# Kernel tuning notes

Measured on AMD Instinct MI355X. Metric: run time of the kernel, lower is better.

## Reference

```python
import jax, jax.numpy as jnp
import numpy as np

ENC_H = 128
DEC_H = 256
DEC_STEPS = 10


def _gru_cell(x, h, Wih, Whh, bih, bhh):
    # PyTorch GRU cell, gate order (r, z, n)
    gi = x @ Wih.T + bih          # (B, 3H)
    gh = h @ Whh.T + bhh          # (B, 3H)
    H = h.shape[-1]
    ir, iz, inn = gi[:, :H], gi[:, H:2 * H], gi[:, 2 * H:]
    hr, hz, hn = gh[:, :H], gh[:, H:2 * H], gh[:, 2 * H:]
    r = jax.nn.sigmoid(ir + hr)
    z = jax.nn.sigmoid(iz + hz)
    n = jnp.tanh(inn + r * hn)
    return (1.0 - z) * n + z * h


def setup_inputs() -> dict:
    key = jax.random.key(0)
    ks = jax.random.split(key, 12)
    B, S = 4096, 128
    s = 0.1
    return {
        "x": jax.random.normal(ks[0], (B, S, 5), jnp.float32),
        "y": jax.random.normal(ks[1], (B, S, 1), jnp.float32),
        "enc_Wih": jax.random.normal(ks[2], (3 * ENC_H, 5), jnp.float32) * s,
        "enc_Whh": jax.random.normal(ks[3], (3 * ENC_H, ENC_H), jnp.float32) * s,
        "enc_bih": jax.random.normal(ks[4], (3 * ENC_H,), jnp.float32) * s,
        "enc_bhh": jax.random.normal(ks[5], (3 * ENC_H,), jnp.float32) * s,
        "dec_Wih": jax.random.normal(ks[6], (3 * DEC_H, ENC_H + 1), jnp.float32) * s,
        "dec_Whh": jax.random.normal(ks[7], (3 * DEC_H, DEC_H), jnp.float32) * s,
        "dec_bih": jax.random.normal(ks[8], (3 * DEC_H,), jnp.float32) * s,
        "dec_bhh": jax.random.normal(ks[9], (3 * DEC_H,), jnp.float32) * s,
        "lin_W": jax.random.normal(ks[10], (4, DEC_H), jnp.float32) * s,
        "lin_b": jax.random.normal(ks[11], (4,), jnp.float32) * s,
    }


def reference(x, y, enc_Wih, enc_Whh, enc_bih, enc_bhh,
              dec_Wih, dec_Whh, dec_bih, dec_bhh, lin_W, lin_b):
    B, S, _ = x.shape
    xs = jnp.transpose(x, (1, 0, 2))   # (S, B, 5)
    ys = jnp.transpose(y, (1, 0, 2))   # (S, B, 1)

    # Encoder: only the final hidden state (contex) is consumed downstream.
    h0 = jnp.zeros((B, ENC_H), x.dtype)

    def enc_step(h, xt):
        return _gru_cell(xt, h, enc_Wih, enc_Whh, enc_bih, enc_bhh), None

    contex, _ = jax.lax.scan(enc_step, h0, xs)   # (B, 128)

    # Decoder: initial hidden is ones (torch.ones_like(shape)), 10 steps.
    hdec0 = jnp.ones((B, DEC_H), x.dtype)

    def dec_step(h, yt):
        xt = jnp.concatenate([contex, yt], axis=-1)   # (B, 129)
        h2 = _gru_cell(xt, h, dec_Wih, dec_Whh, dec_bih, dec_bhh)
        out = h2 @ lin_W.T + lin_b                    # (B, 4)
        return h2, out

    _, outs = jax.lax.scan(dec_step, hdec0, ys[:DEC_STEPS])  # (10, B, 4)

    # res starts as ones; only first 10 rows written.
    res = jnp.ones((S, B, 4), x.dtype).at[:DEC_STEPS].set(outs)
    return jnp.transpose(res, (1, 0, 2))   # (B, S, 4)
```

## Files before the change

### kernel.cpp

```cpp
#include <hip/hip_runtime.h>

#define B_SZ 4096
#define S_SZ 128
#define XD 5
#define EH 128
#define DH 256
#define DSTEPS 10

typedef short v8s __attribute__((ext_vector_type(8)));
typedef float v4f __attribute__((ext_vector_type(4)));

__device__ __forceinline__ float bf2f(unsigned short u) {
    union { unsigned int i; float f; } v; v.i = ((unsigned int)u) << 16; return v.f;
}
__device__ __forceinline__ unsigned short f2bf(float f) {
    union { float f; unsigned int i; } v; v.f = f;
    unsigned int x = v.i;
    return (unsigned short)((x + 0x7FFFu + ((x >> 16) & 1u)) >> 16);
}
__device__ __forceinline__ float fexp2(float x) { return __builtin_amdgcn_exp2f(x); }
__device__ __forceinline__ float frcp(float x) { return __builtin_amdgcn_rcpf(x); }
__device__ __forceinline__ unsigned int cvt2bf(float lo, float hi) {
    unsigned int r;
    asm("v_cvt_pk_bf16_f32 %0, %1, %2" : "=v"(r) : "v"(lo), "v"(hi));
    return r;
}

#define SC_S (-1.44269504088896f)
#define SC_T ( 2.88539008177793f)

__global__ __launch_bounds__(256) void prep_kernel(
    const float* __restrict__ dWih,
    const float* __restrict__ dWhh,
    unsigned short* __restrict__ wihp,
    unsigned short* __restrict__ dWhh_bf)
{
    const int gsz = gridDim.x * 256;
    for (int i = blockIdx.x * 256 + threadIdx.x; i < 768 * 256; i += gsz) {
        const float sc = ((i >> 8) < 512) ? SC_S : SC_T;
        dWhh_bf[i] = f2bf(sc * dWhh[i]);
    }
    for (int i = blockIdx.x * 256 + threadIdx.x; i < 768 * 136; i += gsz) {
        int col = i / 136, k = i - col * 136;
        const float sc = (col < 512) ? SC_S : SC_T;
        wihp[i] = (k < 129) ? f2bf(sc * dWih[col * 129 + k]) : (unsigned short)0;
    }
}

__global__ __launch_bounds__(1024)
void fused_kernel(
    const float* __restrict__ x,
    const float* __restrict__ Wih32,
    const float* __restrict__ Whh32,
    const float* __restrict__ bih,
    const float* __restrict__ bhh,
    const float* __restrict__ dbih,
    const float* __restrict__ dbhh,
    const float* __restrict__ y,
    const unsigned short* __restrict__ wihp,
    const unsigned short* __restrict__ dWhh_bf,
    const float* __restrict__ linW,
    const float* __restrict__ linb,
    float* __restrict__ out)
{
    __shared__ __align__(16) char uni[118784];
    __shared__ unsigned short hb[2][16][136];
    __shared__ __align__(16) unsigned short zpad[8];
    __shared__ unsigned short hshf[32 * 16 * 8];
    __shared__ unsigned short lwf[32 * 16 * 8];
    __shared__ float ysh[16][DSTEPS];

    const int tid = threadIdx.x;
    const int bid = blockIdx.x;
    const int wv = tid >> 6;
    const int lane = tid & 63;
    const int n = lane & 15;
    const int kg = lane >> 4;
    const int r0 = bid * 16;

    {
        auto xs = (unsigned short (*)[16][8])uni;

        for (int i = tid; i < 2 * 16 * 136; i += 1024) ((unsigned short*)hb)[i] = 0;
        if (tid < 8) zpad[tid] = 0;
        for (int i = tid; i < 16 * S_SZ * 8; i += 1024) {
            int m = i >> 10;
            int rem = i & 1023;
            int t = rem >> 3;
            int j = rem & 7;
            unsigned short v = 0;
            if (j < XD) v = f2bf(x[(size_t)(r0 + m) * (S_SZ * XD) + t * XD + j]);
            else if (j == XD) v = 0x3F80;
            xs[t][m][j] = v;
        }

        const int colw = wv * 16 + n;
        v8s fw[3][4];
        v8s fx[3];
        float bhn = 0.f;
        if (wv < 8) {
            #pragma unroll
            for (int g = 0; g < 3; ++g) {
                const float sc = (g < 2) ? SC_S : SC_T;
                const int gcol = g * EH + colw;
                #pragma unroll
                for (int kt = 0; kt < 4; ++kt) {
                    const float* p = &Whh32[(size_t)gcol * EH + kt * 32 + kg * 8];
                    float4 lo = *(const float4*)p;
                    float4 hi = *(const float4*)(p + 4);
                    v8s f;
                    f[0] = (short)f2bf(sc * lo.x); f[1] = (short)f2bf(sc * lo.y);
                    f[2] = (short)f2bf(sc * lo.z); f[3] = (short)f2bf(sc * lo.w);
                    f[4] = (short)f2bf(sc * hi.x); f[5] = (short)f2bf(sc * hi.y);
                    f[6] = (short)f2bf(sc * hi.z); f[7] = (short)f2bf(sc * hi.w);
                    fw[g][kt] = f;
                }
                v8s t = {0, 0, 0, 0, 0, 0, 0, 0};
                if (kg == 0) {
                    const float* p = &Wih32[gcol * XD];
                    #pragma unroll
                    for (int j = 0; j < XD; ++j) t[j] = (short)f2bf(sc * p[j]);
                    float b = (g < 2) ? (sc * (bih[gcol] + bhh[gcol]))
                                      : (sc * bih[gcol]);
                    t[XD] = (short)f2bf(b);
                }
                fx[g] = t;
            }
            bhn = SC_T * bhh[2 * EH + colw];
        }

        const v4f vzero = {0.f, 0.f, 0.f, 0.f};
        float hst[4] = {0.f, 0.f, 0.f, 0.f};
        __syncthreads();

        #pragma unroll 2
        for (int t = 0; t < S_SZ; ++t) {
            const int p = t & 1;
            if (wv < 8) {
                v8s a[4];
                #pragma unroll
                for (int kt = 0; kt < 4; ++kt)
                    a[kt] = *(const v8s*)&hb[p][n][kt * 32 + kg * 8];
                const unsigned short* xsrc = (kg == 0) ? &xs[t][n][0] : &zpad[0];
                v8s ax = *(const v8s*)xsrc;

                v4f accr  = __builtin_amdgcn_mfma_f32_16x16x32_bf16(a[0], fw[0][0], vzero, 0, 0, 0);
                v4f accz  = __builtin_amdgcn_mfma_f32_16x16x32_bf16(a[0], fw[1][0], vzero, 0, 0, 0);
                v4f acchn = __builtin_amdgcn_mfma_f32_16x16x32_bf16(a[0], fw[2][0], vzero, 0, 0, 0);
                #pragma unroll
                for (int kt = 1; kt < 4; ++kt) {
                    accr  = __builtin_amdgcn_mfma_f32_16x16x32_bf16(a[kt], fw[0][kt], accr, 0, 0, 0);
                    accz  = __builtin_amdgcn_mfma_f32_16x16x32_bf16(a[kt], fw[1][kt], accz, 0, 0, 0);
                    acchn = __builtin_amdgcn_mfma_f32_16x16x32_bf16(a[kt], fw[2][kt], acchn, 0, 0, 0);
                }
                accr = __builtin_amdgcn_mfma_f32_16x16x32_bf16(ax, fx[0], accr, 0, 0, 0);
                accz = __builtin_amdgcn_mfma_f32_16x16x32_bf16(ax, fx[1], accz, 0, 0, 0);
                v4f accin = __builtin_amdgcn_mfma_f32_16x16x32_bf16(ax, fx[2], vzero, 0, 0, 0);

                float hnew[4];
                #pragma unroll
                for (int e = 0; e < 4; ++e) {
                    float r  = frcp(1.f + fexp2(accr[e]));
                    float z  = frcp(1.f + fexp2(accz[e]));
                    float nn = 1.f - 2.f * frcp(fexp2(accin[e] + r * (acchn[e] + bhn)) + 1.f);
                    float h  = nn + z * (hst[e] - nn);
                    hst[e] = h;
                    hnew[e] = h;
                }
                const unsigned int pk01 = cvt2bf(hnew[0], hnew[1]);
                const unsigned int pk23 = cvt2bf(hnew[2], hnew[3]);
                hb[1 - p][kg * 4 + 0][colw] = (unsigned short)(pk01 & 0xFFFFu);
                hb[1 - p][kg * 4 + 1][colw] = (unsigned short)(pk01 >> 16);
                hb[1 - p][kg * 4 + 2][colw] = (unsigned short)(pk23 & 0xFFFFu);
                hb[1 - p][kg * 4 + 3][colw] = (unsigned short)(pk23 >> 16);
            }
            __syncthreads();
        }
    }

    {
        const int w = wv;
        const int colb = w * 16;
        const int rb = r0;
        float* gwsh = (float*)uni;

        if (tid < 512) {
            int col = tid >> 5, kgrp = tid & 31;
            unsigned short v8[8];
            #pragma unroll
            for (int j = 0; j < 8; ++j)
                v8[j] = (col < 4) ? f2bf(linW[col * 256 + kgrp * 8 + j]) : (unsigned short)0;
            *(uint4*)&lwf[(kgrp * 16 + col) * 8] = *(uint4*)v8;
        }
        if (tid < 16 * DSTEPS) {
            int row = tid / DSTEPS, tt = tid - row * DSTEPS;
            ysh[row][tt] = y[(size_t)(rb + row) * S_SZ + tt];
        }
        for (int i = tid; i < 32 * 16 * 8; i += 1024) hshf[i] = 0x3F80;

        v8s fB[3][8];
        #pragma unroll
        for (int g = 0; g < 3; ++g)
            #pragma unroll
            for (int kt = 0; kt < 8; ++kt)
                fB[g][kt] = *(const v8s*)
                    &dWhh_bf[(size_t)(g * DH + colb + n) * DH + kt * 32 + kg * 8];

        const v4f vzero = {0.f, 0.f, 0.f, 0.f};
        v4f gi[3];
        #pragma unroll
        for (int g = 0; g < 3; ++g) gi[g] = vzero;

        #pragma unroll
        for (int kt = 0; kt < 4; ++kt) {
            v8s actex = *(const v8s*)&hb[0][n][kt * 32 + kg * 8];
            #pragma unroll
            for (int g = 0; g < 3; ++g) {
                v8s bw = *(const v8s*)
                    &wihp[(size_t)(g * DH + colb + n) * 136 + kt * 32 + kg * 8];
                gi[g] = __builtin_amdgcn_mfma_f32_16x16x32_bf16(bw, actex, gi[g], 0, 0, 0);
            }
        }

        #pragma unroll
        for (int g = 0; g < 3; ++g) {
            const float sc = (g < 2) ? SC_S : SC_T;
            #pragma unroll
            for (int e = 0; e < 4; ++e) {
                const int gcol = g * DH + colb + kg * 4 + e;
                gi[g][e] += sc * (dbih[gcol] + ((g < 2) ? dbhh[gcol] : 0.f));
                gwsh[tid * 29 + 12 + g * 4 + e] = bf2f(wihp[(size_t)gcol * 136 + 128]);
            }
            *(v4f*)&gwsh[tid * 29 + g * 4] = gi[g];
        }
        #pragma unroll
        for (int e = 0; e < 4; ++e)
            gwsh[tid * 29 + 24 + e] = SC_T * dbhh[2 * DH + colb + kg * 4 + e];

        float hprev[4] = {1.f, 1.f, 1.f, 1.f};
        __syncthreads();

        for (int t = 0; t < DSTEPS; ++t) {
            const float yv = ysh[n][t];

            v4f ar = vzero, az = vzero, an = vzero;
            #pragma unroll
            for (int kt = 0; kt < 8; ++kt) {
                v8s a = *(const v8s*)&hshf[((kt * 4 + kg) * 16 + n) * 8];
                ar = __builtin_amdgcn_mfma_f32_16x16x32_bf16(fB[0][kt], a, ar, 0, 0, 0);
                az = __builtin_amdgcn_mfma_f32_16x16x32_bf16(fB[1][kt], a, az, 0, 0, 0);
                an = __builtin_amdgcn_mfma_f32_16x16x32_bf16(fB[2][kt], a, an, 0, 0, 0);
            }
            __syncthreads();

            float hh[4];
            #pragma unroll
            for (int e = 0; e < 4; ++e) {
                const float giR = gwsh[tid * 29 + 0 + e];
                const float giZ = gwsh[tid * 29 + 4 + e];
                const float giN = gwsh[tid * 29 + 8 + e];
                const float wyR = gwsh[tid * 29 + 12 + e];
                const float wyZ = gwsh[tid * 29 + 16 + e];
                const float wyN = gwsh[tid * 29 + 20 + e];
                const float bN  = gwsh[tid * 29 + 24 + e];
                float r  = frcp(1.f + fexp2(giR + yv * wyR + ar[e]));
                float z  = frcp(1.f + fexp2(giZ + yv * wyZ + az[e]));
                float nn = 1.f - 2.f * frcp(
                    fexp2(giN + yv * wyN + r * (an[e] + bN)) + 1.f);
                float h  = nn + z * (hprev[e] - nn);
                hprev[e] = h;
                hh[e] = h;
            }
            const unsigned int p01 = cvt2bf(hh[0], hh[1]);
            const unsigned int p23 = cvt2bf(hh[2], hh[3]);
            const int base = colb + kg * 4;
            const int idx = (((base >> 3) * 16) + n) * 8 + (base & 7);
            *(uint2*)&hshf[idx] = (uint2){p01, p23};
            __syncthreads();

            if (w == t) {
                v4f o4 = vzero;
                #pragma unroll
                for (int kt = 0; kt < 8; ++kt) {
                    v8s a = *(const v8s*)&hshf[((kt * 4 + kg) * 16 + n) * 8];
                    v8s b = *(const v8s*)&lwf[((kt * 4 + kg) * 16 + n) * 8];
                    o4 = __builtin_amdgcn_mfma_f32_16x16x32_bf16(b, a, o4, 0, 0, 0);
                }
                if (kg == 0) {
                    const float4 lb4 = *(const float4*)linb;
                    float4 ov = {o4[0] + lb4.x, o4[1] + lb4.y, o4[2] + lb4.z, o4[3] + lb4.w};
                    *(float4*)&out[(size_t)(rb + n) * (S_SZ * 4) + t * 4] = ov;
                }
            }
        }

        for (int j = tid; j < 16 * 512; j += 1024) {
            int row = j >> 9, c = j & 511;
            if (c >= DSTEPS * 4) out[(size_t)(rb + row) * 512 + c] = 1.0f;
        }
    }
}

extern "C" void kernel_launch(void* const* d_in, const int* in_sizes, int n_in,
                              void* d_out, int out_size, void* d_ws, size_t ws_size,
                              hipStream_t stream)
{
    const float* x    = (const float*)d_in[0];
    const float* y    = (const float*)d_in[1];
    const float* eWih = (const float*)d_in[2];
    const float* eWhh = (const float*)d_in[3];
    const float* ebih = (const float*)d_in[4];
    const float* ebhh = (const float*)d_in[5];
    const float* dWih = (const float*)d_in[6];
    const float* dWhh = (const float*)d_in[7];
    const float* dbih = (const float*)d_in[8];
    const float* dbhh = (const float*)d_in[9];
    const float* linW = (const float*)d_in[10];
    const float* linb = (const float*)d_in[11];
    float* out = (float*)d_out;

    char* ws = (char*)d_ws;
    unsigned short* wihp    = (unsigned short*)(ws);
    unsigned short* dWhh_bf = (unsigned short*)(ws + 208896);

    prep_kernel<<<256, 256, 0, stream>>>(dWih, dWhh, wihp, dWhh_bf);
    fused_kernel<<<256, 1024, 0, stream>>>(x, eWih, eWhh, ebih, ebhh,
                                           dbih, dbhh, y, wihp, dWhh_bf,
                                           linW, linb, out);
}
```

Baseline: 208.1 us.

## Split fused encoder/decoder into separate 512-thread encoder and decoder kernels

The encoder now runs in its own 512-thread kernel, so the 8 idle waves of the 1024-thread block no longer wait at every one of the 128 per-step barriers. The decoder weight preparation is folded into the encoder kernel, which removes the separate prep launch. The encoder writes the context to global memory in bf16 for the decoder kernel to read. In exchange the decoder becomes a second launch and adds a global round trip for the context, and the encoder kernel's register and LDS limits differ from before.

```diff
diff --git a/kernel.cpp b/kernel.cpp
--- a/kernel.cpp
+++ b/kernel.cpp
@@ -29,46 +29,21 @@
 #define SC_S (-1.44269504088896f)
 #define SC_T ( 2.88539008177793f)
 
-__global__ __launch_bounds__(256) void prep_kernel(
-    const float* __restrict__ dWih,
-    const float* __restrict__ dWhh,
-    unsigned short* __restrict__ wihp,
-    unsigned short* __restrict__ dWhh_bf)
-{
-    const int gsz = gridDim.x * 256;
-    for (int i = blockIdx.x * 256 + threadIdx.x; i < 768 * 256; i += gsz) {
-        const float sc = ((i >> 8) < 512) ? SC_S : SC_T;
-        dWhh_bf[i] = f2bf(sc * dWhh[i]);
-    }
-    for (int i = blockIdx.x * 256 + threadIdx.x; i < 768 * 136; i += gsz) {
-        int col = i / 136, k = i - col * 136;
-        const float sc = (col < 512) ? SC_S : SC_T;
-        wihp[i] = (k < 129) ? f2bf(sc * dWih[col * 129 + k]) : (unsigned short)0;
-    }
-}
-
-__global__ __launch_bounds__(1024)
-void fused_kernel(
+__global__ __launch_bounds__(512) void enc_kernel(
     const float* __restrict__ x,
     const float* __restrict__ Wih32,
     const float* __restrict__ Whh32,
     const float* __restrict__ bih,
     const float* __restrict__ bhh,
-    const float* __restrict__ dbih,
-    const float* __restrict__ dbhh,
-    const float* __restrict__ y,
-    const unsigned short* __restrict__ wihp,
-    const unsigned short* __restrict__ dWhh_bf,
-    const float* __restrict__ linW,
-    const float* __restrict__ linb,
-    float* __restrict__ out)
+    const float* __restrict__ dWih,
+    const float* __restrict__ dWhh,
+    unsigned short* __restrict__ wihp,
+    unsigned short* __restrict__ dWhh_bf,
+    unsigned short* __restrict__ ctex)
 {
-    __shared__ __align__(16) char uni[118784];
+    __shared__ unsigned short xs[S_SZ][16][8];
     __shared__ unsigned short hb[2][16][136];
     __shared__ __align__(16) unsigned short zpad[8];
-    __shared__ unsigned short hshf[32 * 16 * 8];
-    __shared__ unsigned short lwf[32 * 16 * 8];
-    __shared__ float ysh[16][DSTEPS];
 
     const int tid = threadIdx.x;
     const int bid = blockIdx.x;
@@ -78,226 +53,249 @@
     const int kg = lane >> 4;
     const int r0 = bid * 16;
 
-    {
-        auto xs = (unsigned short (*)[16][8])uni;
-
-        for (int i = tid; i < 2 * 16 * 136; i += 1024) ((unsigned short*)hb)[i] = 0;
-        if (tid < 8) zpad[tid] = 0;
-        for (int i = tid; i < 16 * S_SZ * 8; i += 1024) {
-            int m = i >> 10;
-            int rem = i & 1023;
-            int t = rem >> 3;
-            int j = rem & 7;
-            unsigned short v = 0;
-            if (j < XD) v = f2bf(x[(size_t)(r0 + m) * (S_SZ * XD) + t * XD + j]);
-            else if (j == XD) v = 0x3F80;
-            xs[t][m][j] = v;
-        }
-
-        const int colw = wv * 16 + n;
-        v8s fw[3][4];
-        v8s fx[3];
-        float bhn = 0.f;
-        if (wv < 8) {
+    for (int i = bid * 512 + tid; i < 768 * 256; i += 131072) {
+        const float sc = ((i >> 8) < 512) ? SC_S : SC_T;
+        dWhh_bf[i] = f2bf(sc * dWhh[i]);
+    }
+    for (int i = bid * 512 + tid; i < 768 * 136; i += 131072) {
+        int col = i / 136, k = i - col * 136;
+        const float sc = (col < 512) ? SC_S : SC_T;
+        wihp[i] = (k < 129) ? f2bf(sc * dWih[col * 129 + k]) : (unsigned short)0;
+    }
+
+    for (int i = tid; i < 2 * 16 * 136; i += 512) ((unsigned short*)hb)[i] = 0;
+    if (tid < 8) zpad[tid] = 0;
+    for (int i = tid; i < 16 * S_SZ * 8; i += 512) {
+        int m = i >> 10;
+        int rem = i & 1023;
+        int t = rem >> 3;
+        int j = rem & 7;
+        unsigned short v = 0;
+        if (j < XD) v = f2bf(x[(size_t)(r0 + m) * (S_SZ * XD) + t * XD + j]);
+        else if (j == XD) v = 0x3F80;
+        xs[t][m][j] = v;
+    }
+
+    const int colw = wv * 16 + n;
+    v8s fw[3][4];
+    v8s fx[3];
+    #pragma unroll
+    for (int g = 0; g < 3; ++g) {
+        const float sc = (g < 2) ? SC_S : SC_T;
+        const int gcol = g * EH + colw;
+        #pragma unroll
+        for (int kt = 0; kt < 4; ++kt) {
+            const float* p = &Whh32[(size_t)gcol * EH + kt * 32 + kg * 8];
+            float4 lo = *(const float4*)p;
+            float4 hi = *(const float4*)(p + 4);
+            v8s f;
+            f[0] = (short)f2bf(sc * lo.x); f[1] = (short)f2bf(sc * lo.y);
+            f[2] = (short)f2bf(sc * lo.z); f[3] = (short)f2bf(sc * lo.w);
+            f[4] = (short)f2bf(sc * hi.x); f[5] = (short)f2bf(sc * hi.y);
+            f[6] = (short)f2bf(sc * hi.z); f[7] = (short)f2bf(sc * hi.w);
+            fw[g][kt] = f;
+        }
+        v8s t = {0, 0, 0, 0, 0, 0, 0, 0};
+        if (kg == 0) {
+            const float* p = &Wih32[gcol * XD];
             #pragma unroll
-            for (int g = 0; g < 3; ++g) {
-                const float sc = (g < 2) ? SC_S : SC_T;
-                const int gcol = g * EH + colw;
-                #pragma unroll
-                for (int kt = 0; kt < 4; ++kt) {
-                    const float* p = &Whh32[(size_t)gcol * EH + kt * 32 + kg * 8];
-                    float4 lo = *(const float4*)p;
-                    float4 hi = *(const float4*)(p + 4);
-                    v8s f;
-                    f[0] = (short)f2bf(sc * lo.x); f[1] = (short)f2bf(sc * lo.y);
-                    f[2] = (short)f2bf(sc * lo.z); f[3] = (short)f2bf(sc * lo.w);
-                    f[4] = (short)f2bf(sc * hi.x); f[5] = (short)f2bf(sc * hi.y);
-                    f[6] = (short)f2bf(sc * hi.z); f[7] = (short)f2bf(sc * hi.w);
-                    fw[g][kt] = f;
-                }
-                v8s t = {0, 0, 0, 0, 0, 0, 0, 0};
-                if (kg == 0) {
-                    const float* p = &Wih32[gcol * XD];
-                    #pragma unroll
-                    for (int j = 0; j < XD; ++j) t[j] = (short)f2bf(sc * p[j]);
-                    float b = (g < 2) ? (sc * (bih[gcol] + bhh[gcol]))
-                                      : (sc * bih[gcol]);
-                    t[XD] = (short)f2bf(b);
-                }
-                fx[g] = t;
-            }
-            bhn = SC_T * bhh[2 * EH + colw];
-        }
-
-        const v4f vzero = {0.f, 0.f, 0.f, 0.f};
-        float hst[4] = {0.f, 0.f, 0.f, 0.f};
+            for (int j = 0; j < XD; ++j) t[j] = (short)f2bf(sc * p[j]);
+            float b = (g < 2) ? (sc * (bih[gcol] + bhh[gcol]))
+                              : (sc * bih[gcol]);
+            t[XD] = (short)f2bf(b);
+        }
+        fx[g] = t;
+    }
+    const float bhn = SC_T * bhh[2 * EH + colw];
+
+    const v4f vzero = {0.f, 0.f, 0.f, 0.f};
+    float hst[4] = {0.f, 0.f, 0.f, 0.f};
+    __syncthreads();
+
+    #pragma unroll 2
+    for (int t = 0; t < S_SZ; ++t) {
+        const int p = t & 1;
+        v8s a[4];
+        #pragma unroll
+        for (int kt = 0; kt < 4; ++kt)
+            a[kt] = *(const v8s*)&hb[p][n][kt * 32 + kg * 8];
+        const unsigned short* xsrc = (kg == 0) ? &xs[t][n][0] : &zpad[0];
+        v8s ax = *(const v8s*)xsrc;
+
+        v4f accr  = __builtin_amdgcn_mfma_f32_16x16x32_bf16(a[0], fw[0][0], vzero, 0, 0, 0);
+        v4f accz  = __builtin_amdgcn_mfma_f32_16x16x32_bf16(a[0], fw[1][0], vzero, 0, 0, 0);
+        v4f acchn = __builtin_amdgcn_mfma_f32_16x16x32_bf16(a[0], fw[2][0], vzero, 0, 0, 0);
+        #pragma unroll
+        for (int kt = 1; kt < 4; ++kt) {
+            accr  = __builtin_amdgcn_mfma_f32_16x16x32_bf16(a[kt], fw[0][kt], accr, 0, 0, 0);
+            accz  = __builtin_amdgcn_mfma_f32_16x16x32_bf16(a[kt], fw[1][kt], accz, 0, 0, 0);
+            acchn = __builtin_amdgcn_mfma_f32_16x16x32_bf16(a[kt], fw[2][kt], acchn, 0, 0, 0);
+        }
+        accr = __builtin_amdgcn_mfma_f32_16x16x32_bf16(ax, fx[0], accr, 0, 0, 0);
+        accz = __builtin_amdgcn_mfma_f32_16x16x32_bf16(ax, fx[1], accz, 0, 0, 0);
+        v4f accin = __builtin_amdgcn_mfma_f32_16x16x32_bf16(ax, fx[2], vzero, 0, 0, 0);
+
+        float hnew[4];
+        #pragma unroll
+        for (int e = 0; e < 4; ++e) {
+            float r  = frcp(1.f + fexp2(accr[e]));
+            float z  = frcp(1.f + fexp2(accz[e]));
+            float nn = 1.f - 2.f * frcp(fexp2(accin[e] + r * (acchn[e] + bhn)) + 1.f);
+            float h  = nn + z * (hst[e] - nn);
+            hst[e] = h;
+            hnew[e] = h;
+        }
+        const unsigned int pk01 = cvt2bf(hnew[0], hnew[1]);
+        const unsigned int pk23 = cvt2bf(hnew[2], hnew[3]);
+        hb[1 - p][kg * 4 + 0][colw] = (unsigned short)(pk01 & 0xFFFFu);
+        hb[1 - p][kg * 4 + 1][colw] = (unsigned short)(pk01 >> 16);
+        hb[1 - p][kg * 4 + 2][colw] = (unsigned short)(pk23 & 0xFFFFu);
+        hb[1 - p][kg * 4 + 3][colw] = (unsigned short)(pk23 >> 16);
         __syncthreads();
-
-        #pragma unroll 2
-        for (int t = 0; t < S_SZ; ++t) {
-            const int p = t & 1;
-            if (wv < 8) {
-                v8s a[4];
-                #pragma unroll
-                for (int kt = 0; kt < 4; ++kt)
-                    a[kt] = *(const v8s*)&hb[p][n][kt * 32 + kg * 8];
-                const unsigned short* xsrc = (kg == 0) ? &xs[t][n][0] : &zpad[0];
-                v8s ax = *(const v8s*)xsrc;
-
-                v4f accr  = __builtin_amdgcn_mfma_f32_16x16x32_bf16(a[0], fw[0][0], vzero, 0, 0, 0);
-                v4f accz  = __builtin_amdgcn_mfma_f32_16x16x32_bf16(a[0], fw[1][0], vzero, 0, 0, 0);
-                v4f acchn = __builtin_amdgcn_mfma_f32_16x16x32_bf16(a[0], fw[2][0], vzero, 0, 0, 0);
-                #pragma unroll
-                for (int kt = 1; kt < 4; ++kt) {
-                    accr  = __builtin_amdgcn_mfma_f32_16x16x32_bf16(a[kt], fw[0][kt], accr, 0, 0, 0);
-                    accz  = __builtin_amdgcn_mfma_f32_16x16x32_bf16(a[kt], fw[1][kt], accz, 0, 0, 0);
-                    acchn = __builtin_amdgcn_mfma_f32_16x16x32_bf16(a[kt], fw[2][kt], acchn, 0, 0, 0);
-                }
-                accr = __builtin_amdgcn_mfma_f32_16x16x32_bf16(ax, fx[0], accr, 0, 0, 0);
-                accz = __builtin_amdgcn_mfma_f32_16x16x32_bf16(ax, fx[1], accz, 0, 0, 0);
-                v4f accin = __builtin_amdgcn_mfma_f32_16x16x32_bf16(ax, fx[2], vzero, 0, 0, 0);
-
-                float hnew[4];
-                #pragma unroll
-                for (int e = 0; e < 4; ++e) {
-                    float r  = frcp(1.f + fexp2(accr[e]));
-                    float z  = frcp(1.f + fexp2(accz[e]));
-                    float nn = 1.f - 2.f * frcp(fexp2(accin[e] + r * (acchn[e] + bhn)) + 1.f);
-                    float h  = nn + z * (hst[e] - nn);
-                    hst[e] = h;
-                    hnew[e] = h;
-                }
-                const unsigned int pk01 = cvt2bf(hnew[0], hnew[1]);
-                const unsigned int pk23 = cvt2bf(hnew[2], hnew[3]);
-                hb[1 - p][kg * 4 + 0][colw] = (unsigned short)(pk01 & 0xFFFFu);
-                hb[1 - p][kg * 4 + 1][colw] = (unsigned short)(pk01 >> 16);
-                hb[1 - p][kg * 4 + 2][colw] = (unsigned short)(pk23 & 0xFFFFu);
-                hb[1 - p][kg * 4 + 3][colw] = (unsigned short)(pk23 >> 16);
-            }
-            __syncthreads();
-        }
-    }
-
-    {
-        const int w = wv;
-        const int colb = w * 16;
-        const int rb = r0;
-        float* gwsh = (float*)uni;
-
-        if (tid < 512) {
-            int col = tid >> 5, kgrp = tid & 31;
-            unsigned short v8[8];
-            #pragma unroll
-            for (int j = 0; j < 8; ++j)
-                v8[j] = (col < 4) ? f2bf(linW[col * 256 + kgrp * 8 + j]) : (unsigned short)0;
-            *(uint4*)&lwf[(kgrp * 16 + col) * 8] = *(uint4*)v8;
-        }
-        if (tid < 16 * DSTEPS) {
-            int row = tid / DSTEPS, tt = tid - row * DSTEPS;
-            ysh[row][tt] = y[(size_t)(rb + row) * S_SZ + tt];
-        }
-        for (int i = tid; i < 32 * 16 * 8; i += 1024) hshf[i] = 0x3F80;
-
-        v8s fB[3][8];
-        #pragma unroll
-        for (int g = 0; g < 3; ++g)
-            #pragma unroll
-            for (int kt = 0; kt < 8; ++kt)
-                fB[g][kt] = *(const v8s*)
-                    &dWhh_bf[(size_t)(g * DH + colb + n) * DH + kt * 32 + kg * 8];
-
-        const v4f vzero = {0.f, 0.f, 0.f, 0.f};
-        v4f gi[3];
-        #pragma unroll
-        for (int g = 0; g < 3; ++g) gi[g] = vzero;
-
-        #pragma unroll
-        for (int kt = 0; kt < 4; ++kt) {
-            v8s actex = *(const v8s*)&hb[0][n][kt * 32 + kg * 8];
-            #pragma unroll
-            for (int g = 0; g < 3; ++g) {
-                v8s bw = *(const v8s*)
-                    &wihp[(size_t)(g * DH + colb + n) * 136 + kt * 32 + kg * 8];
-                gi[g] = __builtin_amdgcn_mfma_f32_16x16x32_bf16(bw, actex, gi[g], 0, 0, 0);
-            }
-        }
-
+    }
+    #pragma unroll
+    for (int e = 0; e < 4; ++e)
+        ctex[(size_t)(r0 + kg * 4 + e) * EH + colw] = f2bf(hst[e]);
+}
+
+__global__ __launch_bounds__(1024)
+void dec_all_kernel(
+    const unsigned short* __restrict__ dWhh_bf,
+    const unsigned short* __restrict__ wihp,
+    const float* __restrict__ dbih,
+    const float* __restrict__ dbhh,
+    const float* __restrict__ y,
+    const unsigned short* __restrict__ ctex,
+    const float* __restrict__ linW,
+    const float* __restrict__ linb,
+    float* __restrict__ out)
+{
+    __shared__ float gwsh[1024 * 29];
+    __shared__ unsigned short hshf[32 * 16 * 8];
+    __shared__ unsigned short lwf[32 * 16 * 8];
+    __shared__ float ysh[16][DSTEPS];
+
+    const int tid = threadIdx.x;
+    const int wv = tid >> 6;
+    const int lane = tid & 63;
+    const int n = lane & 15;
+    const int kg = lane >> 4;
+    const int rb = blockIdx.x * 16;
+    const int colb = wv * 16;
+
+    if (tid < 512) {
+        int col = tid >> 5, kgrp = tid & 31;
+        unsigned short v8[8];
+        #pragma unroll
+        for (int j = 0; j < 8; ++j)
+            v8[j] = (col < 4) ? f2bf(linW[col * 256 + kgrp * 8 + j]) : (unsigned short)0;
+        *(uint4*)&lwf[(kgrp * 16 + col) * 8] = *(uint4*)v8;
+    }
+    if (tid < 16 * DSTEPS) {
+        int row = tid / DSTEPS, tt = tid - row * DSTEPS;
+        ysh[row][tt] = y[(size_t)(rb + row) * S_SZ + tt];
+    }
+    for (int i = tid; i < 32 * 16 * 8; i += 1024) hshf[i] = 0x3F80;
+
+    v8s fB[3][8];
+    #pragma unroll
+    for (int g = 0; g < 3; ++g)
+        #pragma unroll
+        for (int kt = 0; kt < 8; ++kt)
+            fB[g][kt] = *(const v8s*)
+                &dWhh_bf[(size_t)(g * DH + colb + n) * DH + kt * 32 + kg * 8];
+
+    const v4f vzero = {0.f, 0.f, 0.f, 0.f};
+    v4f gi[3];
+    #pragma unroll
+    for (int g = 0; g < 3; ++g) gi[g] = vzero;
+
+    #pragma unroll
+    for (int kt = 0; kt < 4; ++kt) {
+        v8s actex = *(const v8s*)&ctex[(size_t)(rb + n) * EH + kt * 32 + kg * 8];
         #pragma unroll
         for (int g = 0; g < 3; ++g) {
-            const float sc = (g < 2) ? SC_S : SC_T;
-            #pragma unroll
-            for (int e = 0; e < 4; ++e) {
-                const int gcol = g * DH + colb + kg * 4 + e;
-                gi[g][e] += sc * (dbih[gcol] + ((g < 2) ? dbhh[gcol] : 0.f));
-                gwsh[tid * 29 + 12 + g * 4 + e] = bf2f(wihp[(size_t)gcol * 136 + 128]);
-            }
-            *(v4f*)&gwsh[tid * 29 + g * 4] = gi[g];
-        }
-        #pragma unroll
-        for (int e = 0; e < 4; ++e)
-            gwsh[tid * 29 + 24 + e] = SC_T * dbhh[2 * DH + colb + kg * 4 + e];
-
-        float hprev[4] = {1.f, 1.f, 1.f, 1.f};
+            v8s bw = *(const v8s*)
+                &wihp[(size_t)(g * DH + colb + n) * 136 + kt * 32 + kg * 8];
+            gi[g] = __builtin_amdgcn_mfma_f32_16x16x32_bf16(bw, actex, gi[g], 0, 0, 0);
+        }
+    }
+
+    #pragma unroll
+    for (int g = 0; g < 3; ++g) {
+        const float sc = (g < 2) ? SC_S : SC_T;
+        #pragma unroll
+        for (int e = 0; e < 4; ++e) {
+            const int gcol = g * DH + colb + kg * 4 + e;
+            gi[g][e] += sc * (dbih[gcol] + ((g < 2) ? dbhh[gcol] : 0.f));
+            gwsh[tid * 29 + 12 + g * 4 + e] = bf2f(wihp[(size_t)gcol * 136 + 128]);
+        }
+        *(v4f*)&gwsh[tid * 29 + g * 4] = gi[g];
+    }
+    #pragma unroll
+    for (int e = 0; e < 4; ++e)
+        gwsh[tid * 29 + 24 + e] = SC_T * dbhh[2 * DH + colb + kg * 4 + e];
+
+    float hprev[4] = {1.f, 1.f, 1.f, 1.f};
+    __syncthreads();
+
+    for (int t = 0; t < DSTEPS; ++t) {
+        const float yv = ysh[n][t];
+
+        v4f ar = vzero, az = vzero, an = vzero;
+        #pragma unroll
+        for (int kt = 0; kt < 8; ++kt) {
+            v8s a = *(const v8s*)&hshf[((kt * 4 + kg) * 16 + n) * 8];
+            ar = __builtin_amdgcn_mfma_f32_16x16x32_bf16(fB[0][kt], a, ar, 0, 0, 0);
+            az = __builtin_amdgcn_mfma_f32_16x16x32_bf16(fB[1][kt], a, az, 0, 0, 0);
+            an = __builtin_amdgcn_mfma_f32_16x16x32_bf16(fB[2][kt], a, an, 0, 0, 0);
+        }
         __syncthreads();
 
-        for (int t = 0; t < DSTEPS; ++t) {
-            const float yv = ysh[n][t];
-
-            v4f ar = vzero, az = vzero, an = vzero;
+        float hh[4];
+        #pragma unroll
+        for (int e = 0; e < 4; ++e) {
+            const float giR = gwsh[tid * 29 + 0 + e];
+            const float giZ = gwsh[tid * 29 + 4 + e];
+            const float giN = gwsh[tid * 29 + 8 + e];
+            const float wyR = gwsh[tid * 29 + 12 + e];
+            const float wyZ = gwsh[tid * 29 + 16 + e];
+            const float wyN = gwsh[tid * 29 + 20 + e];
+            const float bN  = gwsh[tid * 29 + 24 + e];
+            float r  = frcp(1.f + fexp2(giR + yv * wyR + ar[e]));
+            float z  = frcp(1.f + fexp2(giZ + yv * wyZ + az[e]));
+            float nn = 1.f - 2.f * frcp(
+                fexp2(giN + yv * wyN + r * (an[e] + bN)) + 1.f);
+            float h  = nn + z * (hprev[e] - nn);
+            hprev[e] = h;
+            hh[e] = h;
+        }
+        const unsigned int p01 = cvt2bf(hh[0], hh[1]);
+        const unsigned int p23 = cvt2bf(hh[2], hh[3]);
+        const int base = colb + kg * 4;
+        const int idx = (((base >> 3) * 16) + n) * 8 + (base & 7);
+        *(uint2*)&hshf[idx] = (uint2){p01, p23};
+        __syncthreads();
+
+        if (wv == t) {
+            v4f o4 = vzero;
             #pragma unroll
             for (int kt = 0; kt < 8; ++kt) {
                 v8s a = *(const v8s*)&hshf[((kt * 4 + kg) * 16 + n) * 8];
-                ar = __builtin_amdgcn_mfma_f32_16x16x32_bf16(fB[0][kt], a, ar, 0, 0, 0);
-                az = __builtin_amdgcn_mfma_f32_16x16x32_bf16(fB[1][kt], a, az, 0, 0, 0);
-                an = __builtin_amdgcn_mfma_f32_16x16x32_bf16(fB[2][kt], a, an, 0, 0, 0);
+                v8s b = *(const v8s*)&lwf[((kt * 4 + kg) * 16 + n) * 8];
+                o4 = __builtin_amdgcn_mfma_f32_16x16x32_bf16(b, a, o4, 0, 0, 0);
             }
-            __syncthreads();
-
-            float hh[4];
-            #pragma unroll
-            for (int e = 0; e < 4; ++e) {
-                const float giR = gwsh[tid * 29 + 0 + e];
-                const float giZ = gwsh[tid * 29 + 4 + e];
-                const float giN = gwsh[tid * 29 + 8 + e];
-                const float wyR = gwsh[tid * 29 + 12 + e];
-                const float wyZ = gwsh[tid * 29 + 16 + e];
-                const float wyN = gwsh[tid * 29 + 20 + e];
-                const float bN  = gwsh[tid * 29 + 24 + e];
-                float r  = frcp(1.f + fexp2(giR + yv * wyR + ar[e]));
-                float z  = frcp(1.f + fexp2(giZ + yv * wyZ + az[e]));
-                float nn = 1.f - 2.f * frcp(
-                    fexp2(giN + yv * wyN + r * (an[e] + bN)) + 1.f);
-                float h  = nn + z * (hprev[e] - nn);
-                hprev[e] = h;
-                hh[e] = h;
+            if (kg == 0) {
+                const float4 lb4 = *(const float4*)linb;
+                float4 ov = {o4[0] + lb4.x, o4[1] + lb4.y, o4[2] + lb4.z, o4[3] + lb4.w};
+                *(float4*)&out[(size_t)(rb + n) * (S_SZ * 4) + t * 4] = ov;
             }
-            const unsigned int p01 = cvt2bf(hh[0], hh[1]);
-            const unsigned int p23 = cvt2bf(hh[2], hh[3]);
-            const int base = colb + kg * 4;
-            const int idx = (((base >> 3) * 16) + n) * 8 + (base & 7);
-            *(uint2*)&hshf[idx] = (uint2){p01, p23};
-            __syncthreads();
-
-            if (w == t) {
-                v4f o4 = vzero;
-                #pragma unroll
-                for (int kt = 0; kt < 8; ++kt) {
-                    v8s a = *(const v8s*)&hshf[((kt * 4 + kg) * 16 + n) * 8];
-                    v8s b = *(const v8s*)&lwf[((kt * 4 + kg) * 16 + n) * 8];
-                    o4 = __builtin_amdgcn_mfma_f32_16x16x32_bf16(b, a, o4, 0, 0, 0);
-                }
-                if (kg == 0) {
-                    const float4 lb4 = *(const float4*)linb;
-                    float4 ov = {o4[0] + lb4.x, o4[1] + lb4.y, o4[2] + lb4.z, o4[3] + lb4.w};
-                    *(float4*)&out[(size_t)(rb + n) * (S_SZ * 4) + t * 4] = ov;
-                }
-            }
-        }
-
-        for (int j = tid; j < 16 * 512; j += 1024) {
-            int row = j >> 9, c = j & 511;
-            if (c >= DSTEPS * 4) out[(size_t)(rb + row) * 512 + c] = 1.0f;
-        }
+        }
+    }
+
+    for (int j = tid; j < 16 * 512; j += 1024) {
+        int row = j >> 9, c = j & 511;
+        if (c >= DSTEPS * 4) out[(size_t)(rb + row) * 512 + c] = 1.0f;
     }
 }
 
@@ -322,9 +320,10 @@
     char* ws = (char*)d_ws;
     unsigned short* wihp    = (unsigned short*)(ws);
     unsigned short* dWhh_bf = (unsigned short*)(ws + 208896);
-
-    prep_kernel<<<256, 256, 0, stream>>>(dWih, dWhh, wihp, dWhh_bf);
-    fused_kernel<<<256, 1024, 0, stream>>>(x, eWih, eWhh, ebih, ebhh,
-                                           dbih, dbhh, y, wihp, dWhh_bf,
-                                           linW, linb, out);
-}
+    unsigned short* ctex    = (unsigned short*)(ws + 602112);
+
+    enc_kernel<<<256, 512, 0, stream>>>(x, eWih, eWhh, ebih, ebhh,
+                                        dWih, dWhh, wihp, dWhh_bf, ctex);
+    dec_all_kernel<<<256, 1024, 0, stream>>>(dWhh_bf, wihp, dbih, dbhh, y,
+                                             ctex, linW, linb, out);
+}
```

Result: no change. 209.2 us (+0.5%).
